# Optimization experiments

Hardware: AMD Instinct MI355X
Metric: run time of the kernel (lower is better)

## Reference

```python
import jax, jax.numpy as jnp
import numpy as np
from jax import lax

# dims: batch, item seq len, d_model, d_inner, d_state, d_conv, dt_rank, n_layers
B, L, H, E, N, K, R, NL = 256, 200, 256, 512, 16, 4, 16, 2
V = 150000            # int(n_items * 1.5)
USER_ID = 1
T = L + L // 2        # interleaved length
EPS = 1e-12

FLOATS = ('item_emb', 'ln_w', 'ln_b', 'in_proj_w', 'conv_w', 'conv_b', 'x_proj_w',
          'dt_w', 'dt_b', 'A_log', 'Dp', 'out_w', 'mn_w', 'mn_b',
          'fc1_w', 'fc1_b', 'fc2_w', 'fc2_b', 'fn_w', 'fn_b')


def setup_inputs():
    key = jax.random.key(0)
    ks = jax.random.split(key, 12)
    g = lambda k, s: jax.random.normal(k, s, jnp.float32) * 0.02
    return dict(
        item_seq=jax.random.randint(ks[0], (B, L), 0, 100000),
        seq_len=jax.random.randint(ks[1], (B,), 0, 200),
        item_emb=g(ks[2], (V, H)),
        ln_w=jnp.ones((H,)), ln_b=jnp.zeros((H,)),
        in_proj_w=g(ks[3], (NL, 2 * E, H)),
        conv_w=g(ks[4], (NL, E, K)), conv_b=jnp.zeros((NL, E)),
        x_proj_w=g(ks[5], (NL, R + 2 * N, E)),
        dt_w=g(ks[6], (NL, E, R)), dt_b=jnp.zeros((NL, E)),
        A_log=jnp.tile(jnp.log(jnp.arange(1, N + 1, dtype=jnp.float32)), (NL, E, 1)),
        Dp=jnp.ones((NL, E)),
        out_w=g(ks[7], (NL, H, E)),
        mn_w=jnp.ones((NL, H)), mn_b=jnp.zeros((NL, H)),
        fc1_w=g(ks[8], (NL, 4 * H, H)), fc1_b=jnp.zeros((NL, 4 * H)),
        fc2_w=g(ks[9], (NL, H, 4 * H)), fc2_b=jnp.zeros((NL, H)),
        fn_w=jnp.ones((NL, H)), fn_b=jnp.zeros((NL, H)),
    )


def _ln(x, w, b):
    m = x.mean(-1, keepdims=True)
    v = x.var(-1, keepdims=True)
    return (x - m) * lax.rsqrt(v + EPS) * w + b


def _interleave(seq):
    # [B,L] -> [B, L + L//2], user separator after every 2 items
    i = jnp.arange(L)
    out = jnp.zeros((seq.shape[0], T), seq.dtype)
    out = out.at[:, i + i // 2].set(seq)
    io = jnp.arange(1, L, 2)            # odd positions close a pair
    out = out.at[:, io + io // 2 + 1].set(-USER_ID)
    return out


def _selective_scan(xc, dt, Bm, Cm, A, D):
    # xc, dt: [B,T,E]; Bm, Cm: [B,T,N]; A: [E,N]; D: [E]
    def step(s, ins):
        x_t, dt_t, b_t, c_t = ins                     # [B,E],[B,E],[B,N],[B,N]
        s = s * jnp.exp(dt_t[..., None] * A) + (dt_t * x_t)[..., None] * b_t[:, None, :]
        return s, jnp.einsum('ben,bn->be', s, c_t)
    s0 = jnp.zeros((xc.shape[0], E, N), xc.dtype)
    xs = tuple(a.swapaxes(0, 1) for a in (xc, dt, Bm, Cm))
    _, ys = lax.scan(step, s0, xs)
    return ys.swapaxes(0, 1) + xc * D


def _mamba(x, p):
    xz = x @ p['in_proj_w'].T                         # [B,T,2E]
    xc, z = jnp.split(xz, 2, axis=-1)
    xcT = lax.conv_general_dilated(xc.swapaxes(1, 2), p['conv_w'][:, None, :], (1,),
                                   [(K - 1, 0)], dimension_numbers=('NCH', 'OIH', 'NCH'),
                                   feature_group_count=E)
    xc = jax.nn.silu(xcT + p['conv_b'][None, :, None]).swapaxes(1, 2)  # causal depthwise conv
    xdbl = xc @ p['x_proj_w'].T                       # [B,T,R+2N]
    dt = jax.nn.softplus(xdbl[..., :R] @ p['dt_w'].T + p['dt_b'])
    Bm, Cm = xdbl[..., R:R + N], xdbl[..., R + N:]
    y = _selective_scan(xc, dt, Bm, Cm, -jnp.exp(p['A_log']), p['Dp'])
    return (y * jax.nn.silu(z)) @ p['out_w'].T


def _core(item_seq, seq_len, F):
    tot = _interleave(item_seq)
    tot = jnp.where(tot < 0, tot + V, tot)            # negative user id wraps into table
    h = _ln(F['item_emb'][tot], F['ln_w'], F['ln_b'])  # dropout is identity (eval)
    per = ('in_proj_w', 'conv_w', 'conv_b', 'x_proj_w', 'dt_w', 'dt_b', 'A_log', 'Dp', 'out_w')
    for l in range(NL):
        p = {k: F[k][l] for k in per}
        h = _ln(_mamba(h, p) + h, F['mn_w'][l], F['mn_b'][l])   # use_residual=True (NL>1)
        ff = jax.nn.gelu(h @ F['fc1_w'][l].T + F['fc1_b'][l], approximate=False)
        ff = ff @ F['fc2_w'][l].T + F['fc2_b'][l]
        h = _ln(ff + h, F['fn_w'][l], F['fn_b'][l])
    tl = seq_len + seq_len // 2
    idx = jnp.clip(tl - 1, 0, T - 1)
    return h[jnp.arange(h.shape[0]), idx]             # gather last valid position


def reference(item_seq, seq_len, item_emb, ln_w, ln_b, in_proj_w, conv_w, conv_b,
              x_proj_w, dt_w, dt_b, A_log, Dp, out_w, mn_w, mn_b,
              fc1_w, fc1_b, fc2_w, fc2_b, fn_w, fn_b):
    F = dict(zip(FLOATS, (item_emb, ln_w, ln_b, in_proj_w, conv_w, conv_b, x_proj_w,
                          dt_w, dt_b, A_log, Dp, out_w, mn_w, mn_b,
                          fc1_w, fc1_b, fc2_w, fc2_b, fn_w, fn_b)))
    return _core(item_seq, seq_len, F)
```

## Files before the change

kernel.cpp:

```cpp
#include <hip/hip_runtime.h>
#include <math.h>

typedef unsigned short u16;
typedef __attribute__((ext_vector_type(8))) short bf8_t;
typedef __attribute__((ext_vector_type(4))) float f4_t;

#define BB 256
#define LL 200
#define HH 256
#define EE 512
#define NSTATE 16
#define KCONV 4
#define RR 16
#define NLAYER 2
#define VV 150000
#define TT 300
#define MTOK (BB*TT)
#define NC 6
#define CL 50
#define XW 1024

#define LOG2E 1.44269504088896340736f
#define LN2   0.69314718055994530942f

__device__ __forceinline__ float geluf(float x) {
    return 0.5f * x * (1.0f + erff(x * 0.70710678118654752440f));
}
__device__ __forceinline__ u16 f2bf(float x) {
    unsigned u = __float_as_uint(x);
    unsigned r = u + 0x7FFF + ((u >> 16) & 1);
    return (u16)(r >> 16);
}
__device__ __forceinline__ float bf2f(u16 b) { return __uint_as_float((unsigned)b << 16); }

__device__ __forceinline__ void gload16(const void* gp, void* lp) {
    __builtin_amdgcn_global_load_lds(
        (const __attribute__((address_space(1))) unsigned int*)gp,
        (__attribute__((address_space(3))) unsigned int*)lp,
        16, 0, 0);
}

__device__ __forceinline__ void block_reduce2(float& a, float& b) {
    __shared__ float ra[4], rb[4];
    #pragma unroll
    for (int o = 32; o > 0; o >>= 1) {
        a += __shfl_down(a, o, 64);
        b += __shfl_down(b, o, 64);
    }
    int lane = threadIdx.x & 63, w = threadIdx.x >> 6;
    if (lane == 0) { ra[w] = a; rb[w] = b; }
    __syncthreads();
    a = ra[0] + ra[1] + ra[2] + ra[3];
    b = rb[0] + rb[1] + rb[2] + rb[3];
}

__global__ __launch_bounds__(256)
void split_kernel(const float* __restrict__ x, u16* __restrict__ ph,
                  u16* __restrict__ pl, int n) {
    int i = blockIdx.x * 256 + threadIdx.x;
    if (i < n) {
        float v = x[i];
        u16 hb = f2bf(v);
        ph[i] = hb;
        pl[i] = f2bf(v - bf2f(hb));
    }
}

__global__ __launch_bounds__(256)
void embed_ln_kernel(const int* __restrict__ item_seq,
                     const float* __restrict__ item_emb,
                     const float* __restrict__ ln_w,
                     const float* __restrict__ ln_b,
                     u16* __restrict__ hh, u16* __restrict__ hl) {
    int tok = blockIdx.x;
    int b = tok / TT, p = tok - b * TT;
    int k = p / 3, r = p - 3 * k;
    int item;
    if (r == 2) item = VV - 1;
    else        item = item_seq[b * LL + 2 * k + r];
    int tid = threadIdx.x;
    float x = item_emb[(size_t)item * HH + tid];
    float s1 = x, s2 = x * x;
    block_reduce2(s1, s2);
    float m = s1 * (1.0f / HH);
    float var = s2 * (1.0f / HH) - m * m;
    float inv = rsqrtf(var + 1e-12f);
    float v = (x - m) * inv * ln_w[tid] + ln_b[tid];
    size_t idx = (size_t)tok * HH + tid;
    u16 hb = f2bf(v);
    hh[idx] = hb;
    hl[idx] = f2bf(v - bf2f(hb));
}

__global__ __launch_bounds__(256)
void add_ln_kernel(const float* __restrict__ tmp,
                   u16* __restrict__ hh, u16* __restrict__ hl,
                   const float* __restrict__ w,
                   const float* __restrict__ bnorm) {
    int tok = blockIdx.x;
    int tid = threadIdx.x;
    size_t idx = (size_t)tok * HH + tid;
    float x = tmp[idx] + bf2f(hh[idx]) + bf2f(hl[idx]);
    float s1 = x, s2 = x * x;
    block_reduce2(s1, s2);
    float m = s1 * (1.0f / HH);
    float var = s2 * (1.0f / HH) - m * m;
    float inv = rsqrtf(var + 1e-12f);
    float v = (x - m) * inv * w[tid] + bnorm[tid];
    u16 hb = f2bf(v);
    hh[idx] = hb;
    hl[idx] = f2bf(v - bf2f(hb));
}

template <int MODE>
__global__ __launch_bounds__(256)
void gemm_mfma(const u16* __restrict__ Ah, int ldab,
               const u16* __restrict__ Wh,
               const float* __restrict__ bias,
               float* __restrict__ C, u16* __restrict__ Cb,
               int M, int N, int K, int ldc) {
    __shared__ u16 sA[2][128 * 32];
    __shared__ u16 sB[2][128 * 32];
    int tid = threadIdx.x;
    int lane = tid & 63, wid = tid >> 6;
    int wr = wid >> 1, wc = wid & 1;

    int gx = gridDim.x, nwg = gx * gridDim.y;
    int id = blockIdx.y * gx + blockIdx.x;
    int q = nwg >> 3, rr8 = nwg & 7;
    int xcd = id & 7, pos = id >> 3;
    int nid = (xcd < rr8 ? xcd * (q + 1) : rr8 * (q + 1) + (xcd - rr8) * q) + pos;
    int bn = (nid % gx) * 128;
    int bm = (nid / gx) * 128;

    f4_t acc[4][4];
    #pragma unroll
    for (int i = 0; i < 4; ++i)
        #pragma unroll
        for (int j = 0; j < 4; ++j)
            acc[i][j] = (f4_t){0.f, 0.f, 0.f, 0.f};

    int scol = (lane & 3) * 8;

    auto stageA = [&](int bi, int k0) {
        #pragma unroll
        for (int qq = 0; qq < 2; ++qq) {
            int row = wid * 32 + qq * 16 + (lane >> 2);
            size_t ga = (size_t)(bm + row) * ldab + k0 + scol;
            int off = (wid * 2 + qq) * 1024;
            gload16(Ah + ga, (char*)&sA[bi][0] + off);
        }
    };
    auto stageB = [&](int bi, int k0) {
        #pragma unroll
        for (int qq = 0; qq < 2; ++qq) {
            int row = wid * 32 + qq * 16 + (lane >> 2);
            size_t gb = (size_t)(bn + row) * K + k0 + scol;
            int off = (wid * 2 + qq) * 1024;
            gload16(Wh + gb, (char*)&sB[bi][0] + off);
        }
    };
    auto compute = [&](int bi) {
        int arow = wr * 64 + (lane & 15);
        int koff = (lane >> 4) * 8;
        bf8_t ah[4];
        #pragma unroll
        for (int fm = 0; fm < 4; ++fm) {
            int r = arow + fm * 16;
            ah[fm] = *(const bf8_t*)&sA[bi][r * 32 + koff];
        }
        #pragma unroll
        for (int fn = 0; fn < 4; ++fn) {
            int r = wc * 64 + fn * 16 + (lane & 15);
            bf8_t bh = *(const bf8_t*)&sB[bi][r * 32 + koff];
            #pragma unroll
            for (int fm = 0; fm < 4; ++fm)
                acc[fm][fn] = __builtin_amdgcn_mfma_f32_16x16x32_bf16(ah[fm], bh, acc[fm][fn], 0, 0, 0);
        }
    };

    stageA(0, 0);
    stageB(0, 0);
    __syncthreads();
    int cur = 0;
    for (int k0 = 0; k0 < K; k0 += 32) {
        if (k0 + 32 < K) {
            stageA(cur ^ 1, k0 + 32);
            stageB(cur ^ 1, k0 + 32);
        }
        compute(cur);
        __syncthreads();
        cur ^= 1;
    }

    if (MODE == 2 || MODE == 3) {
        u16* rs = (u16*)&sA[0][0];
        #pragma unroll
        for (int fn = 0; fn < 4; ++fn) {
            int cl = wc * 64 + fn * 16 + (lane & 15);
            float bv = (bias != nullptr) ? bias[bn + cl] : 0.f;
            #pragma unroll
            for (int fm = 0; fm < 4; ++fm) {
                #pragma unroll
                for (int j = 0; j < 4; ++j) {
                    int lr = wr * 64 + fm * 16 + (lane >> 4) * 4 + j;
                    float v = acc[fm][fn][j] + bv;
                    if (MODE == 2) v = geluf(v);
                    rs[lr * 128 + cl] = f2bf(v);
                }
            }
        }
        __syncthreads();
        int r = tid >> 1, half = tid & 1;
        u16* dst = Cb + (size_t)(bm + r) * ldc + bn + half * 64;
        const u16* src = rs + r * 128 + half * 64;
        #pragma unroll
        for (int i = 0; i < 8; ++i)
            *(bf8_t*)&dst[i * 8] = *(const bf8_t*)&src[i * 8];
    } else {
        #pragma unroll
        for (int fn = 0; fn < 4; ++fn) {
            int colg = bn + wc * 64 + fn * 16 + (lane & 15);
            if (colg < N) {
                float bv = (bias != nullptr) ? bias[colg] : 0.f;
                #pragma unroll
                for (int fm = 0; fm < 4; ++fm) {
                    #pragma unroll
                    for (int j = 0; j < 4; ++j) {
                        int rowg = bm + wr * 64 + fm * 16 + (lane >> 4) * 4 + j;
                        C[(size_t)rowg * ldc + colg] = acc[fm][fn][j] + bv;
                    }
                }
            }
        }
    }
}

__global__ __launch_bounds__(256)
void gemm_xproj(const u16* __restrict__ Axz,
                const u16* __restrict__ Wh, const u16* __restrict__ Wl,
                float* __restrict__ C) {
    __shared__ u16 sA[2][128 * 32];
    __shared__ u16 sB[2][2][48 * 32];
    int tid = threadIdx.x;
    int lane = tid & 63, wid = tid >> 6;
    int bm = blockIdx.x * 128;

    f4_t acc[2][3];
    #pragma unroll
    for (int i = 0; i < 2; ++i)
        #pragma unroll
        for (int j = 0; j < 3; ++j)
            acc[i][j] = (f4_t){0.f, 0.f, 0.f, 0.f};

    int scol = (lane & 3) * 8;

    auto stage = [&](int bi, int k0) {
        #pragma unroll
        for (int qq = 0; qq < 2; ++qq) {
            int row = wid * 32 + qq * 16 + (lane >> 2);
            size_t ga = (size_t)(bm + row) * XW + k0 + scol;
            int off = (wid * 2 + qq) * 1024;
            gload16(Axz + ga, (char*)&sA[bi][0] + off);
        }
        if (tid < 192) {
            int row = tid >> 2;
            int c16 = (tid & 3) * 8;
            size_t gb = (size_t)row * EE + k0 + c16;
            gload16(Wh + gb, (char*)&sB[bi][0][0] + tid * 16);
            gload16(Wl + gb, (char*)&sB[bi][1][0] + tid * 16);
        }
    };
    auto compute = [&](int bi) {
        int arow = wid * 32 + (lane & 15);
        int koff = (lane >> 4) * 8;
        bf8_t ah[2];
        #pragma unroll
        for (int fm = 0; fm < 2; ++fm) {
            int r = arow + fm * 16;
            ah[fm] = *(const bf8_t*)&sA[bi][r * 32 + koff];
        }
        #pragma unroll
        for (int fn = 0; fn < 3; ++fn) {
            int r = fn * 16 + (lane & 15);
            bf8_t bh = *(const bf8_t*)&sB[bi][0][r * 32 + koff];
            bf8_t bl = *(const bf8_t*)&sB[bi][1][r * 32 + koff];
            #pragma unroll
            for (int fm = 0; fm < 2; ++fm) {
                acc[fm][fn] = __builtin_amdgcn_mfma_f32_16x16x32_bf16(ah[fm], bh, acc[fm][fn], 0, 0, 0);
                acc[fm][fn] = __builtin_amdgcn_mfma_f32_16x16x32_bf16(ah[fm], bl, acc[fm][fn], 0, 0, 0);
            }
        }
    };

    stage(0, 0);
    __syncthreads();
    int cur = 0;
    for (int k0 = 0; k0 < EE; k0 += 32) {
        if (k0 + 32 < EE) stage(cur ^ 1, k0 + 32);
        compute(cur);
        __syncthreads();
        cur ^= 1;
    }

    #pragma unroll
    for (int fn = 0; fn < 3; ++fn) {
        int colg = fn * 16 + (lane & 15);
        #pragma unroll
        for (int fm = 0; fm < 2; ++fm) {
            #pragma unroll
            for (int j = 0; j < 4; ++j) {
                int rowg = bm + wid * 32 + fm * 16 + (lane >> 4) * 4 + j;
                C[(size_t)rowg * 48 + colg] = acc[fm][fn][j];
            }
        }
    }
}

__global__ __launch_bounds__(256)
void conv_halo_kernel(const u16* __restrict__ xzb, float* __restrict__ halo) {
    int bid = blockIdx.x;
    int ehalf = bid & 1, bc = bid >> 1;
    int c = bc % NC, b = bc / NC;
    int e = ehalf * 256 + threadIdx.x;
    int t0 = c * CL;
    const u16* xp = xzb + (size_t)b * TT * XW + e;
    float* hp = halo + (((size_t)b * NC + c) * 3) * EE + e;
    #pragma unroll
    for (int k = 0; k < 3; ++k) {
        int t = t0 - 3 + k;
        hp[(size_t)k * EE] = (t >= 0) ? bf2f(xp[(size_t)t * XW]) : 0.f;
    }
}

__global__ __launch_bounds__(256)
void conv_chunk_kernel(u16* __restrict__ xzb, const float* __restrict__ halo,
                       const float* __restrict__ conv_w,
                       const float* __restrict__ conv_b, int layer) {
    int bid = blockIdx.x;
    int ehalf = bid & 1, bc = bid >> 1;
    int c = bc % NC, b = bc / NC;
    int e = ehalf * 256 + threadIdx.x;
    int t0 = c * CL;
    const float* w = conv_w + ((size_t)layer * EE + e) * KCONV;
    float w0 = w[0], w1 = w[1], w2 = w[2], w3 = w[3];
    float bias = conv_b[layer * EE + e];
    const float* hp = halo + (((size_t)b * NC + c) * 3) * EE + e;
    float h0 = hp[0], h1 = hp[(size_t)EE], h2 = hp[(size_t)2 * EE];
    u16* p = xzb + ((size_t)b * TT + t0) * XW + e;

    float c0 = bf2f(p[0]);
    float c1 = bf2f(p[(size_t)XW]);
    for (int tg = 0; tg < CL; tg += 2) {
        float n0, n1;
        if (tg + 2 < CL) {
            n0 = bf2f(p[(size_t)(tg + 2) * XW]);
            n1 = bf2f(p[(size_t)(tg + 3) * XW]);
        }
        float v0 = fmaf(w0, h0, fmaf(w1, h1, fmaf(w2, h2, fmaf(w3, c0, bias))));
        float v1 = fmaf(w0, h1, fmaf(w1, h2, fmaf(w2, c0, fmaf(w3, c1, bias))));
        p[(size_t)(tg + 0) * XW] = f2bf(v0 / (1.f + __expf(-v0)));
        p[(size_t)(tg + 1) * XW] = f2bf(v1 / (1.f + __expf(-v1)));
        h0 = h2; h1 = c0; h2 = c1;
        if (tg + 2 < CL) { c0 = n0; c1 = n1; }
    }
}

__device__ __forceinline__ bool chain_check(const float* __restrict__ alp,
                                            float& A0l2e) {
    float a0 = -expf(alp[0]);
    bool ch = true;
    #pragma unroll
    for (int n = 1; n < 16; ++n) {
        float an = -expf(alp[n]);
        ch = ch && (fabsf(an - (n + 1) * a0) <= 1e-3f * (n + 1) * fabsf(a0));
    }
    A0l2e = a0 * LOG2E;
    return ch;
}

template <bool CHAIN, bool EMIT>
__device__ __forceinline__ void scan2_body(
        const float* __restrict__ rowp,
        u16* __restrict__ xp,
        const float dw[2][16], const float db[2],
        const float A0[2], const float (*arl)[16],
        const float Dv[2], float2 (*s2)[8], float* dsum) {
    unsigned xcur = *(const unsigned*)xp;
    unsigned zcur = 0;
    if (EMIT) zcur = *(const unsigned*)(xp + EE);
    for (int t = 0; t < CL; ++t) {
        unsigned xnxt = 0, znxt = 0;
        if (t + 1 < CL) {
            xnxt = *(const unsigned*)(xp + (size_t)(t + 1) * XW);
            if (EMIT) znxt = *(const unsigned*)(xp + (size_t)(t + 1) * XW + EE);
        }
        const float* row = rowp + (size_t)t * 48;
        float2 rw[8], Bv[8], Cv[8];
        #pragma unroll
        for (int j = 0; j < 8; ++j) {
            rw[j] = *(const float2*)(row + 2 * j);
            Bv[j] = *(const float2*)(row + 16 + 2 * j);
            if (EMIT) Cv[j] = *(const float2*)(row + 32 + 2 * j);
        }
        unsigned uout = 0;
        #pragma unroll
        for (int v = 0; v < 2; ++v) {
            float r0 = db[v], r1 = 0.f;
            #pragma unroll
            for (int j = 0; j < 8; ++j) {
                r0 = fmaf(rw[j].x, dw[v][2 * j], r0);
                r1 = fmaf(rw[j].y, dw[v][2 * j + 1], r1);
            }
            float rr = r0 + r1;
            float qv = exp2f(-fabsf(rr) * LOG2E);
            float dt = fmaxf(rr, 0.f) + LN2 * __log2f(1.f + qv);
            if (!EMIT) dsum[v] += dt;
            float xv = bf2f((u16)(v == 0 ? (xcur & 0xffffu) : (xcur >> 16)));
            float dx = dt * xv;
            float2 P[8];
            if (CHAIN) {
                float w1 = exp2f(dt * A0[v]);
                float w2 = w1 * w1;
                float2 w2v = make_float2(w2, w2);
                P[0] = make_float2(w1, w2);
                #pragma unroll
                for (int k = 1; k < 8; ++k) P[k] = P[k - 1] * w2v;
            } else {
                #pragma unroll
                for (int k = 0; k < 8; ++k)
                    P[k] = make_float2(exp2f(dt * arl[v][2 * k]),
                                       exp2f(dt * arl[v][2 * k + 1]));
            }
            float2 dx2 = make_float2(dx, dx);
            float2 qa = make_float2(0.f, 0.f), qb = make_float2(0.f, 0.f);
            #pragma unroll
            for (int k = 0; k < 8; ++k) {
                s2[v][k] = s2[v][k] * P[k] + dx2 * Bv[k];
                if (EMIT) {
                    if (k & 1) qb += s2[v][k] * Cv[k];
                    else       qa += s2[v][k] * Cv[k];
                }
            }
            if (EMIT) {
                float2 qs = qa + qb;
                float y = (qs.x + qs.y) + xv * Dv[v];
                float zv = bf2f((u16)(v == 0 ? (zcur & 0xffffu) : (zcur >> 16)));
                float u = y * (zv / (1.f + __expf(-zv)));
                uout |= (unsigned)f2bf(u) << (16 * v);
            }
        }
        if (EMIT) *(unsigned*)(xp + (size_t)t * XW) = uout;
        xcur = xnxt; zcur = znxt;
    }
}

__device__ __forceinline__ void load_scan2_params(
        const float* dt_w, const float* dt_b, const float* A_log,
        int layer, int e0, float dw[2][16], float db[2], float A0[2],
        bool& chain) {
    chain = true;
    #pragma unroll
    for (int v = 0; v < 2; ++v) {
        int e = e0 + v;
        #pragma unroll
        for (int i = 0; i < 16; i += 4)
            *(float4*)&dw[v][i] = *(const float4*)(dt_w + ((size_t)layer * EE + e) * RR + i);
        db[v] = dt_b[layer * EE + e];
        float a0;
        bool c = chain_check(A_log + ((size_t)layer * EE + e) * NSTATE, a0);
        A0[v] = a0;
        chain = chain && c;
    }
}

__device__ __forceinline__ void load_arl2(const float* A_log, int layer, int e0,
                                          float arl[2][16]) {
    #pragma unroll
    for (int v = 0; v < 2; ++v) {
        const float* alp = A_log + ((size_t)layer * EE + e0 + v) * NSTATE;
        #pragma unroll
        for (int i = 0; i < 16; i += 4) {
            float4 x4 = *(const float4*)(alp + i);
            arl[v][i + 0] = -expf(x4.x) * LOG2E;
            arl[v][i + 1] = -expf(x4.y) * LOG2E;
            arl[v][i + 2] = -expf(x4.z) * LOG2E;
            arl[v][i + 3] = -expf(x4.w) * LOG2E;
        }
    }
}

__global__ __launch_bounds__(256, 1)
void scan_p1(const float* __restrict__ xdbl, u16* __restrict__ xzb,
             const float* __restrict__ dt_w, const float* __restrict__ dt_b,
             const float* __restrict__ A_log,
             float* __restrict__ SF, float* __restrict__ DS, int layer) {
    int bid = blockIdx.x;
    int c = bid % NC, b = bid / NC;
    int e0 = threadIdx.x * 2;
    int t0 = c * CL;
    float dw[2][16], db[2], A0[2];
    bool chain;
    load_scan2_params(dt_w, dt_b, A_log, layer, e0, dw, db, A0, chain);

    const float* rowp = xdbl + ((size_t)b * TT + t0) * 48;
    u16* xp = xzb + ((size_t)b * TT + t0) * XW + e0;
    float2 s2[2][8];
    #pragma unroll
    for (int v = 0; v < 2; ++v)
        #pragma unroll
        for (int k = 0; k < 8; ++k) s2[v][k] = make_float2(0.f, 0.f);
    float dsum[2] = {0.f, 0.f};
    float Dv[2] = {0.f, 0.f};
    if (chain) {
        scan2_body<true, false>(rowp, xp, dw, db, A0, nullptr, Dv, s2, dsum);
    } else {
        float arl[2][16];
        load_arl2(A_log, layer, e0, arl);
        scan2_body<false, false>(rowp, xp, dw, db, A0, arl, Dv, s2, dsum);
    }
    #pragma unroll
    for (int v = 0; v < 2; ++v) {
        size_t sbase = (((size_t)b * EE + e0 + v) * NC + c) * 16;
        #pragma unroll
        for (int k = 0; k < 8; ++k) *(float2*)(SF + sbase + 2 * k) = s2[v][k];
        DS[((size_t)b * EE + e0 + v) * NC + c] = dsum[v];
    }
}

__global__ __launch_bounds__(256)
void scan_p2(const float* __restrict__ A_log,
             float* __restrict__ SF, const float* __restrict__ DS, int layer) {
    int g = blockIdx.x * 256 + threadIdx.x;
    int e = g & (EE - 1), b = g >> 9;
    const float* alp = A_log + ((size_t)layer * EE + e) * NSTATE;
    float arl2e[16];
    #pragma unroll
    for (int i = 0; i < 16; i += 4) {
        float4 v = *(const float4*)(alp + i);
        arl2e[i + 0] = -expf(v.x) * LOG2E; arl2e[i + 1] = -expf(v.y) * LOG2E;
        arl2e[i + 2] = -expf(v.z) * LOG2E; arl2e[i + 3] = -expf(v.w) * LOG2E;
    }
    float s[16];
    #pragma unroll
    for (int n = 0; n < 16; ++n) s[n] = 0.f;
    size_t base = ((size_t)b * EE + e) * NC;
    for (int c = 0; c < NC; ++c) {
        float ds = DS[base + c];
        alignas(16) float f[16];
        #pragma unroll
        for (int i = 0; i < 16; i += 4) *(float4*)&f[i] = *(const float4*)(SF + (base + c) * 16 + i);
        #pragma unroll
        for (int i = 0; i < 16; i += 4) *(float4*)(SF + (base + c) * 16 + i) = *(float4*)&s[i];
        #pragma unroll
        for (int n = 0; n < 16; ++n) s[n] = fmaf(s[n], exp2f(ds * arl2e[n]), f[n]);
    }
}

__global__ __launch_bounds__(256, 1)
void scan_p3(const float* __restrict__ xdbl, u16* __restrict__ xzb,
             const float* __restrict__ dt_w, const float* __restrict__ dt_b,
             const float* __restrict__ A_log, const float* __restrict__ Dp,
             const float* __restrict__ SF, int layer) {
    int bid = blockIdx.x;
    int c = bid % NC, b = bid / NC;
    int e0 = threadIdx.x * 2;
    int t0 = c * CL;
    float dw[2][16], db[2], A0[2];
    bool chain;
    load_scan2_params(dt_w, dt_b, A_log, layer, e0, dw, db, A0, chain);
    float Dv[2];
    Dv[0] = Dp[layer * EE + e0];
    Dv[1] = Dp[layer * EE + e0 + 1];

    const float* rowp = xdbl + ((size_t)b * TT + t0) * 48;
    u16* xp = xzb + ((size_t)b * TT + t0) * XW + e0;
    float2 s2[2][8];
    #pragma unroll
    for (int v = 0; v < 2; ++v) {
        size_t sbase = (((size_t)b * EE + e0 + v) * NC + c) * 16;
        #pragma unroll
        for (int k = 0; k < 8; ++k) s2[v][k] = *(const float2*)(SF + sbase + 2 * k);
    }
    float dsum[2] = {0.f, 0.f};
    if (chain) {
        scan2_body<true, true>(rowp, xp, dw, db, A0, nullptr, Dv, s2, dsum);
    } else {
        float arl[2][16];
        load_arl2(A_log, layer, e0, arl);
        scan2_body<false, true>(rowp, xp, dw, db, A0, arl, Dv, s2, dsum);
    }
}

__global__ __launch_bounds__(256)
void gather_out_kernel(const u16* __restrict__ hh, const u16* __restrict__ hl,
                       const int* __restrict__ seq_len,
                       float* __restrict__ out) {
    int b = blockIdx.x;
    int sl = seq_len[b];
    int tl = sl + sl / 2;
    int idx = tl - 1;
    if (idx < 0) idx = 0;
    if (idx > TT - 1) idx = TT - 1;
    size_t src = ((size_t)b * TT + idx) * HH + threadIdx.x;
    out[(size_t)b * HH + threadIdx.x] = bf2f(hh[src]) + bf2f(hl[src]);
}

extern "C" void kernel_launch(void* const* d_in, const int* in_sizes, int n_in,
                              void* d_out, int out_size, void* d_ws, size_t ws_size,
                              hipStream_t stream) {
    const int*   item_seq  = (const int*)  d_in[0];
    const int*   seq_len   = (const int*)  d_in[1];
    const float* item_emb  = (const float*)d_in[2];
    const float* ln_w      = (const float*)d_in[3];
    const float* ln_b      = (const float*)d_in[4];
    const float* in_proj_w = (const float*)d_in[5];
    const float* conv_w    = (const float*)d_in[6];
    const float* conv_b    = (const float*)d_in[7];
    const float* x_proj_w  = (const float*)d_in[8];
    const float* dt_w      = (const float*)d_in[9];
    const float* dt_b      = (const float*)d_in[10];
    const float* A_log     = (const float*)d_in[11];
    const float* Dp        = (const float*)d_in[12];
    const float* out_w     = (const float*)d_in[13];
    const float* mn_w      = (const float*)d_in[14];
    const float* mn_b      = (const float*)d_in[15];
    const float* fc1_w     = (const float*)d_in[16];
    const float* fc1_b     = (const float*)d_in[17];
    const float* fc2_w     = (const float*)d_in[18];
    const float* fc2_b     = (const float*)d_in[19];
    const float* fn_w      = (const float*)d_in[20];
    const float* fn_b      = (const float*)d_in[21];

    u16*   xzb  = (u16*)d_ws;
    u16*   hh   = xzb + (size_t)MTOK * XW;
    u16*   hl   = hh + (size_t)MTOK * HH;
    float* tmp  = (float*)(hl + (size_t)MTOK * HH);
    float* xdbl = tmp;
    float* SF   = tmp + (size_t)3686400;
    float* DS   = tmp + (size_t)16269312;
    float* halo = tmp + (size_t)17055744;
    u16* pw   = (u16*)(tmp + (size_t)MTOK * HH);
    u16* inH  = pw;                 u16* inL  = inH  + 524288;
    u16* xpH  = inL  + 524288;      u16* xpL  = xpH  + 49152;
    u16* outH = xpL  + 49152;       u16* outL = outH + 262144;
    u16* f1H  = outL + 262144;      u16* f1L  = f1H  + 524288;
    u16* f2H  = f1L  + 524288;      u16* f2L  = f2H  + 524288;
    u16* ffb = xzb;

    split_kernel<<<524288 / 256, 256, 0, stream>>>(in_proj_w, inH, inL, 524288);
    split_kernel<<<49152 / 256, 256, 0, stream>>>(x_proj_w, xpH, xpL, 49152);
    split_kernel<<<262144 / 256, 256, 0, stream>>>(out_w, outH, outL, 262144);
    split_kernel<<<524288 / 256, 256, 0, stream>>>(fc1_w, f1H, f1L, 524288);
    split_kernel<<<524288 / 256, 256, 0, stream>>>(fc2_w, f2H, f2L, 524288);

    embed_ln_kernel<<<MTOK, 256, 0, stream>>>(item_seq, item_emb, ln_w, ln_b, hh, hl);

    const int gconv = BB * NC * 2;
    const int gscan = BB * NC;

    for (int l = 0; l < NLAYER; ++l) {
        {
            dim3 grid((2 * EE) / 128, MTOK / 128);
            gemm_mfma<3><<<grid, 256, 0, stream>>>(
                hh, HH,
                inH + (size_t)l * 262144,
                nullptr, nullptr, xzb, MTOK, 2 * EE, HH, XW);
        }
        conv_halo_kernel<<<gconv, 256, 0, stream>>>(xzb, halo);
        conv_chunk_kernel<<<gconv, 256, 0, stream>>>(xzb, halo, conv_w, conv_b, l);
        gemm_xproj<<<MTOK / 128, 256, 0, stream>>>(
            xzb, xpH + (size_t)l * 24576, xpL + (size_t)l * 24576, xdbl);
        scan_p1<<<gscan, 256, 0, stream>>>(xdbl, xzb, dt_w, dt_b, A_log, SF, DS, l);
        scan_p2<<<(BB * EE) / 256, 256, 0, stream>>>(A_log, SF, DS, l);
        scan_p3<<<gscan, 256, 0, stream>>>(xdbl, xzb, dt_w, dt_b, A_log, Dp, SF, l);
        {
            dim3 grid(HH / 128, MTOK / 128);
            gemm_mfma<0><<<grid, 256, 0, stream>>>(
                xzb, XW,
                outH + (size_t)l * 131072,
                nullptr, tmp, nullptr, MTOK, HH, EE, HH);
        }
        add_ln_kernel<<<MTOK, 256, 0, stream>>>(tmp, hh, hl, mn_w + l * HH, mn_b + l * HH);
        {
            dim3 grid((4 * HH) / 128, MTOK / 128);
            gemm_mfma<2><<<grid, 256, 0, stream>>>(
                hh, HH,
                f1H + (size_t)l * 262144,
                fc1_b + (size_t)l * 4 * HH,
                nullptr, ffb, MTOK, 4 * HH, HH, XW);
        }
        {
            dim3 grid(HH / 128, MTOK / 128);
            gemm_mfma<0><<<grid, 256, 0, stream>>>(
                ffb, XW,
                f2H + (size_t)l * 262144,
                fc2_b + (size_t)l * HH,
                tmp, nullptr, MTOK, HH, 4 * HH, HH);
        }
        add_ln_kernel<<<MTOK, 256, 0, stream>>>(tmp, hh, hl, fn_w + l * HH, fn_b + l * HH);
    }

    gather_out_kernel<<<BB, 256, 0, stream>>>(hh, hl, seq_len, (float*)d_out);
}
```

Measured before the change: 1.636 ms.

## Store GEMM outputs as bf16, cache dt from scan pass, rechunk scan

The out-proj and fc2 GEMMs now write bf16 through an LDS-staged coalesced store instead of scattered fp32 stores, and add_ln reads bf16. Scan pass 1 computes softplus(dt) once, stores it as bf16, and pass 3 reads it back instead of recomputing the dt projection. The scan chunking changes from 6x50 to 10x30 for more parallelism. These cut memory traffic and recompute but add a bf16 rounding of the residual-branch outputs, an extra dt buffer write/read, and a larger scan state-combine step.

```diff
diff --git a/kernel.cpp b/kernel.cpp
--- a/kernel.cpp
+++ b/kernel.cpp
@@ -16,8 +16,8 @@
 #define VV 150000
 #define TT 300
 #define MTOK (BB*TT)
-#define NC 6
-#define CL 50
+#define NC 10
+#define CL 30
 #define XW 1024
 
 #define LOG2E 1.44269504088896340736f
@@ -93,14 +93,14 @@
 }
 
 __global__ __launch_bounds__(256)
-void add_ln_kernel(const float* __restrict__ tmp,
+void add_ln_kernel(const u16* __restrict__ tmpb,
                    u16* __restrict__ hh, u16* __restrict__ hl,
                    const float* __restrict__ w,
                    const float* __restrict__ bnorm) {
     int tok = blockIdx.x;
     int tid = threadIdx.x;
     size_t idx = (size_t)tok * HH + tid;
-    float x = tmp[idx] + bf2f(hh[idx]) + bf2f(hl[idx]);
+    float x = bf2f(tmpb[idx]) + bf2f(hh[idx]) + bf2f(hl[idx]);
     float s1 = x, s2 = x * x;
     block_reduce2(s1, s2);
     float m = s1 * (1.0f / HH);
@@ -117,7 +117,7 @@
 void gemm_mfma(const u16* __restrict__ Ah, int ldab,
                const u16* __restrict__ Wh,
                const float* __restrict__ bias,
-               float* __restrict__ C, u16* __restrict__ Cb,
+               u16* __restrict__ Cb,
                int M, int N, int K, int ldc) {
     __shared__ u16 sA[2][128 * 32];
     __shared__ u16 sB[2][128 * 32];
@@ -193,47 +193,29 @@
         cur ^= 1;
     }
 
-    if (MODE == 2 || MODE == 3) {
-        u16* rs = (u16*)&sA[0][0];
-        #pragma unroll
-        for (int fn = 0; fn < 4; ++fn) {
-            int cl = wc * 64 + fn * 16 + (lane & 15);
-            float bv = (bias != nullptr) ? bias[bn + cl] : 0.f;
+    u16* rs = (u16*)&sA[0][0];
+    #pragma unroll
+    for (int fn = 0; fn < 4; ++fn) {
+        int cl = wc * 64 + fn * 16 + (lane & 15);
+        float bv = (bias != nullptr) ? bias[bn + cl] : 0.f;
+        #pragma unroll
+        for (int fm = 0; fm < 4; ++fm) {
             #pragma unroll
-            for (int fm = 0; fm < 4; ++fm) {
-                #pragma unroll
-                for (int j = 0; j < 4; ++j) {
-                    int lr = wr * 64 + fm * 16 + (lane >> 4) * 4 + j;
-                    float v = acc[fm][fn][j] + bv;
-                    if (MODE == 2) v = geluf(v);
-                    rs[lr * 128 + cl] = f2bf(v);
-                }
+            for (int j = 0; j < 4; ++j) {
+                int lr = wr * 64 + fm * 16 + (lane >> 4) * 4 + j;
+                float v = acc[fm][fn][j] + bv;
+                if (MODE == 2) v = geluf(v);
+                rs[lr * 128 + cl] = f2bf(v);
             }
         }
-        __syncthreads();
-        int r = tid >> 1, half = tid & 1;
-        u16* dst = Cb + (size_t)(bm + r) * ldc + bn + half * 64;
-        const u16* src = rs + r * 128 + half * 64;
-        #pragma unroll
-        for (int i = 0; i < 8; ++i)
-            *(bf8_t*)&dst[i * 8] = *(const bf8_t*)&src[i * 8];
-    } else {
-        #pragma unroll
-        for (int fn = 0; fn < 4; ++fn) {
-            int colg = bn + wc * 64 + fn * 16 + (lane & 15);
-            if (colg < N) {
-                float bv = (bias != nullptr) ? bias[colg] : 0.f;
-                #pragma unroll
-                for (int fm = 0; fm < 4; ++fm) {
-                    #pragma unroll
-                    for (int j = 0; j < 4; ++j) {
-                        int rowg = bm + wr * 64 + fm * 16 + (lane >> 4) * 4 + j;
-                        C[(size_t)rowg * ldc + colg] = acc[fm][fn][j] + bv;
-                    }
-                }
-            }
-        }
-    }
+    }
+    __syncthreads();
+    int r = tid >> 1, half = tid & 1;
+    u16* dst = Cb + (size_t)(bm + r) * ldc + bn + half * 64;
+    const u16* src = rs + r * 128 + half * 64;
+    #pragma unroll
+    for (int i = 0; i < 8; ++i)
+        *(bf8_t*)&dst[i * 8] = *(const bf8_t*)&src[i * 8];
 }
 
 __global__ __launch_bounds__(256)
@@ -383,6 +365,7 @@
 __device__ __forceinline__ void scan2_body(
         const float* __restrict__ rowp,
         u16* __restrict__ xp,
+        u16* __restrict__ dtp,
         const float dw[2][16], const float db[2],
         const float A0[2], const float (*arl)[16],
         const float Dv[2], float2 (*s2)[8], float* dsum) {
@@ -399,23 +382,33 @@
         float2 rw[8], Bv[8], Cv[8];
         #pragma unroll
         for (int j = 0; j < 8; ++j) {
-            rw[j] = *(const float2*)(row + 2 * j);
+            if (!EMIT) rw[j] = *(const float2*)(row + 2 * j);
             Bv[j] = *(const float2*)(row + 16 + 2 * j);
             if (EMIT) Cv[j] = *(const float2*)(row + 32 + 2 * j);
         }
-        unsigned uout = 0;
+        unsigned dtu = 0;
+        if (EMIT) dtu = *(const unsigned*)(dtp + (size_t)t * EE);
+        unsigned uout = 0, dtout = 0;
         #pragma unroll
         for (int v = 0; v < 2; ++v) {
-            float r0 = db[v], r1 = 0.f;
-            #pragma unroll
-            for (int j = 0; j < 8; ++j) {
-                r0 = fmaf(rw[j].x, dw[v][2 * j], r0);
-                r1 = fmaf(rw[j].y, dw[v][2 * j + 1], r1);
+            float dt;
+            if (!EMIT) {
+                float r0 = db[v], r1 = 0.f;
+                #pragma unroll
+                for (int j = 0; j < 8; ++j) {
+                    r0 = fmaf(rw[j].x, dw[v][2 * j], r0);
+                    r1 = fmaf(rw[j].y, dw[v][2 * j + 1], r1);
+                }
+                float rr = r0 + r1;
+                float qv = exp2f(-fabsf(rr) * LOG2E);
+                float dtf = fmaxf(rr, 0.f) + LN2 * __log2f(1.f + qv);
+                u16 dtb16 = f2bf(dtf);
+                dtout |= (unsigned)dtb16 << (16 * v);
+                dt = bf2f(dtb16);
+                dsum[v] += dt;
+            } else {
+                dt = bf2f((u16)(v == 0 ? (dtu & 0xffffu) : (dtu >> 16)));
             }
-            float rr = r0 + r1;
-            float qv = exp2f(-fabsf(rr) * LOG2E);
-            float dt = fmaxf(rr, 0.f) + LN2 * __log2f(1.f + qv);
-            if (!EMIT) dsum[v] += dt;
             float xv = bf2f((u16)(v == 0 ? (xcur & 0xffffu) : (xcur >> 16)));
             float dx = dt * xv;
             float2 P[8];
@@ -450,25 +443,19 @@
                 uout |= (unsigned)f2bf(u) << (16 * v);
             }
         }
+        if (!EMIT) *(unsigned*)(dtp + (size_t)t * EE) = dtout;
         if (EMIT) *(unsigned*)(xp + (size_t)t * XW) = uout;
         xcur = xnxt; zcur = znxt;
     }
 }
 
-__device__ __forceinline__ void load_scan2_params(
-        const float* dt_w, const float* dt_b, const float* A_log,
-        int layer, int e0, float dw[2][16], float db[2], float A0[2],
-        bool& chain) {
+__device__ __forceinline__ void load_A_params(
+        const float* A_log, int layer, int e0, float A0[2], bool& chain) {
     chain = true;
     #pragma unroll
     for (int v = 0; v < 2; ++v) {
-        int e = e0 + v;
-        #pragma unroll
-        for (int i = 0; i < 16; i += 4)
-            *(float4*)&dw[v][i] = *(const float4*)(dt_w + ((size_t)layer * EE + e) * RR + i);
-        db[v] = dt_b[layer * EE + e];
         float a0;
-        bool c = chain_check(A_log + ((size_t)layer * EE + e) * NSTATE, a0);
+        bool c = chain_check(A_log + ((size_t)layer * EE + e0 + v) * NSTATE, a0);
         A0[v] = a0;
         chain = chain && c;
     }
@@ -492,6 +479,7 @@
 
 __global__ __launch_bounds__(256, 1)
 void scan_p1(const float* __restrict__ xdbl, u16* __restrict__ xzb,
+             u16* __restrict__ dtb,
              const float* __restrict__ dt_w, const float* __restrict__ dt_b,
              const float* __restrict__ A_log,
              float* __restrict__ SF, float* __restrict__ DS, int layer) {
@@ -501,10 +489,19 @@
     int t0 = c * CL;
     float dw[2][16], db[2], A0[2];
     bool chain;
-    load_scan2_params(dt_w, dt_b, A_log, layer, e0, dw, db, A0, chain);
+    #pragma unroll
+    for (int v = 0; v < 2; ++v) {
+        int e = e0 + v;
+        #pragma unroll
+        for (int i = 0; i < 16; i += 4)
+            *(float4*)&dw[v][i] = *(const float4*)(dt_w + ((size_t)layer * EE + e) * RR + i);
+        db[v] = dt_b[layer * EE + e];
+    }
+    load_A_params(A_log, layer, e0, A0, chain);
 
     const float* rowp = xdbl + ((size_t)b * TT + t0) * 48;
     u16* xp = xzb + ((size_t)b * TT + t0) * XW + e0;
+    u16* dtp = dtb + ((size_t)b * TT + t0) * EE + e0;
     float2 s2[2][8];
     #pragma unroll
     for (int v = 0; v < 2; ++v)
@@ -513,11 +510,11 @@
     float dsum[2] = {0.f, 0.f};
     float Dv[2] = {0.f, 0.f};
     if (chain) {
-        scan2_body<true, false>(rowp, xp, dw, db, A0, nullptr, Dv, s2, dsum);
+        scan2_body<true, false>(rowp, xp, dtp, dw, db, A0, nullptr, Dv, s2, dsum);
     } else {
         float arl[2][16];
         load_arl2(A_log, layer, e0, arl);
-        scan2_body<false, false>(rowp, xp, dw, db, A0, arl, Dv, s2, dsum);
+        scan2_body<false, false>(rowp, xp, dtp, dw, db, A0, arl, Dv, s2, dsum);
     }
     #pragma unroll
     for (int v = 0; v < 2; ++v) {
@@ -559,22 +556,23 @@
 
 __global__ __launch_bounds__(256, 1)
 void scan_p3(const float* __restrict__ xdbl, u16* __restrict__ xzb,
-             const float* __restrict__ dt_w, const float* __restrict__ dt_b,
+             u16* __restrict__ dtb,
              const float* __restrict__ A_log, const float* __restrict__ Dp,
              const float* __restrict__ SF, int layer) {
     int bid = blockIdx.x;
     int c = bid % NC, b = bid / NC;
     int e0 = threadIdx.x * 2;
     int t0 = c * CL;
-    float dw[2][16], db[2], A0[2];
+    float A0[2];
     bool chain;
-    load_scan2_params(dt_w, dt_b, A_log, layer, e0, dw, db, A0, chain);
+    load_A_params(A_log, layer, e0, A0, chain);
     float Dv[2];
     Dv[0] = Dp[layer * EE + e0];
     Dv[1] = Dp[layer * EE + e0 + 1];
 
     const float* rowp = xdbl + ((size_t)b * TT + t0) * 48;
     u16* xp = xzb + ((size_t)b * TT + t0) * XW + e0;
+    u16* dtp = dtb + ((size_t)b * TT + t0) * EE + e0;
     float2 s2[2][8];
     #pragma unroll
     for (int v = 0; v < 2; ++v) {
@@ -583,12 +581,14 @@
         for (int k = 0; k < 8; ++k) s2[v][k] = *(const float2*)(SF + sbase + 2 * k);
     }
     float dsum[2] = {0.f, 0.f};
+    float dwd[2][16];
+    float dbd[2] = {0.f, 0.f};
     if (chain) {
-        scan2_body<true, true>(rowp, xp, dw, db, A0, nullptr, Dv, s2, dsum);
+        scan2_body<true, true>(rowp, xp, dtp, dwd, dbd, A0, nullptr, Dv, s2, dsum);
     } else {
         float arl[2][16];
         load_arl2(A_log, layer, e0, arl);
-        scan2_body<false, true>(rowp, xp, dw, db, A0, arl, Dv, s2, dsum);
+        scan2_body<false, true>(rowp, xp, dtp, dwd, dbd, A0, arl, Dv, s2, dsum);
     }
 }
 
@@ -635,12 +635,13 @@
     u16*   xzb  = (u16*)d_ws;
     u16*   hh   = xzb + (size_t)MTOK * XW;
     u16*   hl   = hh + (size_t)MTOK * HH;
-    float* tmp  = (float*)(hl + (size_t)MTOK * HH);
-    float* xdbl = tmp;
-    float* SF   = tmp + (size_t)3686400;
-    float* DS   = tmp + (size_t)16269312;
-    float* halo = tmp + (size_t)17055744;
-    u16* pw   = (u16*)(tmp + (size_t)MTOK * HH);
+    u16*   tmpb = hl + (size_t)MTOK * HH;
+    float* xdbl = (float*)(tmpb + (size_t)MTOK * HH);
+    float* SF   = xdbl + (size_t)MTOK * 48;
+    float* DS   = SF + (size_t)BB * EE * NC * 16;
+    float* halo = DS + (size_t)BB * EE * NC;
+    u16*   dtb  = (u16*)(halo + (size_t)BB * NC * 3 * EE);
+    u16*   pw   = dtb + (size_t)MTOK * EE;
     u16* inH  = pw;                 u16* inL  = inH  + 524288;
     u16* xpH  = inL  + 524288;      u16* xpL  = xpH  + 49152;
     u16* outH = xpL  + 49152;       u16* outL = outH + 262144;
@@ -665,40 +666,40 @@
             gemm_mfma<3><<<grid, 256, 0, stream>>>(
                 hh, HH,
                 inH + (size_t)l * 262144,
-                nullptr, nullptr, xzb, MTOK, 2 * EE, HH, XW);
+                nullptr, xzb, MTOK, 2 * EE, HH, XW);
         }
         conv_halo_kernel<<<gconv, 256, 0, stream>>>(xzb, halo);
         conv_chunk_kernel<<<gconv, 256, 0, stream>>>(xzb, halo, conv_w, conv_b, l);
         gemm_xproj<<<MTOK / 128, 256, 0, stream>>>(
             xzb, xpH + (size_t)l * 24576, xpL + (size_t)l * 24576, xdbl);
-        scan_p1<<<gscan, 256, 0, stream>>>(xdbl, xzb, dt_w, dt_b, A_log, SF, DS, l);
+        scan_p1<<<gscan, 256, 0, stream>>>(xdbl, xzb, dtb, dt_w, dt_b, A_log, SF, DS, l);
         scan_p2<<<(BB * EE) / 256, 256, 0, stream>>>(A_log, SF, DS, l);
-        scan_p3<<<gscan, 256, 0, stream>>>(xdbl, xzb, dt_w, dt_b, A_log, Dp, SF, l);
+        scan_p3<<<gscan, 256, 0, stream>>>(xdbl, xzb, dtb, A_log, Dp, SF, l);
         {
             dim3 grid(HH / 128, MTOK / 128);
-            gemm_mfma<0><<<grid, 256, 0, stream>>>(
+            gemm_mfma<3><<<grid, 256, 0, stream>>>(
                 xzb, XW,
                 outH + (size_t)l * 131072,
-                nullptr, tmp, nullptr, MTOK, HH, EE, HH);
-        }
-        add_ln_kernel<<<MTOK, 256, 0, stream>>>(tmp, hh, hl, mn_w + l * HH, mn_b + l * HH);
+                nullptr, tmpb, MTOK, HH, EE, HH);
+        }
+        add_ln_kernel<<<MTOK, 256, 0, stream>>>(tmpb, hh, hl, mn_w + l * HH, mn_b + l * HH);
         {
             dim3 grid((4 * HH) / 128, MTOK / 128);
             gemm_mfma<2><<<grid, 256, 0, stream>>>(
                 hh, HH,
                 f1H + (size_t)l * 262144,
                 fc1_b + (size_t)l * 4 * HH,
-                nullptr, ffb, MTOK, 4 * HH, HH, XW);
+                ffb, MTOK, 4 * HH, HH, XW);
         }
         {
             dim3 grid(HH / 128, MTOK / 128);
-            gemm_mfma<0><<<grid, 256, 0, stream>>>(
+            gemm_mfma<3><<<grid, 256, 0, stream>>>(
                 ffb, XW,
                 f2H + (size_t)l * 262144,
                 fc2_b + (size_t)l * HH,
-                tmp, nullptr, MTOK, HH, 4 * HH, HH);
-        }
-        add_ln_kernel<<<MTOK, 256, 0, stream>>>(tmp, hh, hl, fn_w + l * HH, fn_b + l * HH);
+                tmpb, MTOK, HH, 4 * HH, HH);
+        }
+        add_ln_kernel<<<MTOK, 256, 0, stream>>>(tmpb, hh, hl, fn_w + l * HH, fn_b + l * HH);
     }
 
     gather_out_kernel<<<BB, 256, 0, stream>>>(hh, hl, seq_len, (float*)d_out);
```

Measured after the change: 1.738 ms. +6.2%, slower.
